# Kernel tuning notes

Hardware: AMD Instinct MI355X
Metric: run time of the kernel (lower is better)

Reference implementation:

```python
import jax, jax.numpy as jnp
import numpy as np

B, L, NIN, NHID, NLAYERS = 16, 2048, 1024, 1024, 2


def _gru_step_zero_h(x, W_ih, b_ih, W_hh, b_hh):
    """torch GRU cell with h_prev = 0 (faithful to the module's bug where
    hidden is never updated and starts at zeros).
    r = sigmoid(W_ir x + b_ir + b_hr)
    z = sigmoid(W_iz x + b_iz + b_hz)
    n = tanh(W_in x + b_in + r * b_hn)   # W_hn @ 0 == 0
    h = (1 - z) * n                       # + z * 0
    W_hh is unused because h_prev == 0 (kept as an arg for parity).
    """
    del W_hh
    g = jnp.einsum('blf,hf->blh', x, W_ih) + b_ih  # (B, L, 3H)
    H = b_ih.shape[0] // 3
    gi_r, gi_z, gi_n = g[..., :H], g[..., H:2 * H], g[..., 2 * H:]
    bh_r, bh_z, bh_n = b_hh[:H], b_hh[H:2 * H], b_hh[2 * H:]
    r = jax.nn.sigmoid(gi_r + bh_r)
    z = jax.nn.sigmoid(gi_z + bh_z)
    n = jnp.tanh(gi_n + r * bh_n)
    return (1.0 - z) * n


def setup_inputs() -> dict:
    key = jax.random.key(0)
    ks = jax.random.split(key, 12)
    s_in = 1.0 / np.sqrt(NIN)
    s_h = 1.0 / np.sqrt(NHID)
    inp = {
        'inputs': jax.random.normal(ks[0], (B, L, NIN), dtype=jnp.float32),
        'inputs_mask': jax.random.randint(ks[1], (B, L), 0, 2, dtype=jnp.int32),
        # layer 0 (input size NIN)
        'W_ih0': jax.random.uniform(ks[2], (3 * NHID, NIN), jnp.float32, -s_in, s_in),
        'W_hh0': jax.random.uniform(ks[3], (3 * NHID, NHID), jnp.float32, -s_h, s_h),
        'b_ih0': jax.random.uniform(ks[4], (3 * NHID,), jnp.float32, -s_h, s_h),
        'b_hh0': jax.random.uniform(ks[5], (3 * NHID,), jnp.float32, -s_h, s_h),
        # layer 1 (input size NHID)
        'W_ih1': jax.random.uniform(ks[6], (3 * NHID, NHID), jnp.float32, -s_h, s_h),
        'W_hh1': jax.random.uniform(ks[7], (3 * NHID, NHID), jnp.float32, -s_h, s_h),
        'b_ih1': jax.random.uniform(ks[8], (3 * NHID,), jnp.float32, -s_h, s_h),
        'b_hh1': jax.random.uniform(ks[9], (3 * NHID,), jnp.float32, -s_h, s_h),
    }
    return inp


def reference(inputs, inputs_mask, W_ih0, W_hh0, b_ih0, b_hh0,
              W_ih1, W_hh1, b_ih1, b_hh1):
    # hidden is never updated in the original step(), so every timestep runs
    # the 2-layer GRU one step from zero hidden -> fully parallel over time.
    h1 = _gru_step_zero_h(inputs, W_ih0, b_ih0, W_hh0, b_hh0)   # (B, L, H)
    h2 = _gru_step_zero_h(h1, W_ih1, b_ih1, W_hh1, b_hh1)       # (B, L, H)
    mask = inputs_mask.astype(h2.dtype)[..., None]               # (B, L, 1)
    # output_p * mask + hidden[0] * (1 - mask), with hidden[0] == 0
    out = h2 * mask
    # original returns (steps, b_s, nhid)
    return jnp.transpose(out, (1, 0, 2))
```

## Files before the change

### kernel.cpp

```cpp
#include <hip/hip_runtime.h>
#include <hip/hip_bf16.h>
#include <cstdint>
#include <cstddef>

#define BB 16
#define LL 2048
#define MM (BB * LL)
#define KK 1024
#define HH 1024

typedef __attribute__((ext_vector_type(8))) short bf16x8;
typedef __attribute__((ext_vector_type(4))) float f32x4;

__device__ __forceinline__ unsigned short f2bf(float f) {
    unsigned u = __builtin_bit_cast(unsigned, f);
    u += 0x7fffu + ((u >> 16) & 1u);
    return (unsigned short)(u >> 16);
}

__global__ void cvt_f32_to_bf16(const float* __restrict__ in,
                                unsigned short* __restrict__ out, int n8) {
    int i = blockIdx.x * blockDim.x + threadIdx.x;
    if (i >= n8) return;
    const float4* p = reinterpret_cast<const float4*>(in) + (size_t)i * 2;
    float4 v0 = p[0];
    float4 v1 = p[1];
    union { unsigned short us[8]; uint4 v; } o;
    o.us[0] = f2bf(v0.x); o.us[1] = f2bf(v0.y);
    o.us[2] = f2bf(v0.z); o.us[3] = f2bf(v0.w);
    o.us[4] = f2bf(v1.x); o.us[5] = f2bf(v1.y);
    o.us[6] = f2bf(v1.z); o.us[7] = f2bf(v1.w);
    reinterpret_cast<uint4*>(out)[i] = o.v;
}

__global__ __launch_bounds__(1024) void scan_mask(const int* __restrict__ mask,
                                                  int* __restrict__ rows,
                                                  int* __restrict__ Na) {
    __shared__ int psum[1024];
    const int t = threadIdx.x;
    const int base = t * 32;
    int m[32];
    int cnt = 0;
#pragma unroll
    for (int i = 0; i < 32; ++i) { m[i] = mask[base + i]; cnt += (m[i] != 0); }
    psum[t] = cnt;
    __syncthreads();
    for (int off = 1; off < 1024; off <<= 1) {
        int v = (t >= off) ? psum[t - off] : 0;
        __syncthreads();
        psum[t] += v;
        __syncthreads();
    }
    int offset = psum[t] - cnt;
#pragma unroll
    for (int i = 0; i < 32; ++i) {
        if (m[i]) rows[offset++] = base + i;
    }
    if (t == 1023) *Na = psum[1023];
}

__global__ __launch_bounds__(256) void gather_cvt(const float* __restrict__ x,
                                                  const int* __restrict__ rows,
                                                  const int* __restrict__ Na,
                                                  unsigned short* __restrict__ xbf) {
    const int j = blockIdx.x;
    if (j >= *Na) return;
    const int r = rows[j];
    const float4 v = reinterpret_cast<const float4*>(x + (size_t)r * KK)[threadIdx.x];
    ushort4 o;
    o.x = f2bf(v.x); o.y = f2bf(v.y); o.z = f2bf(v.z); o.w = f2bf(v.w);
    reinterpret_cast<ushort4*>(xbf + (size_t)j * KK)[threadIdx.x] = o;
}

__global__ __launch_bounds__(256) void zero_masked(const int* __restrict__ mask,
                                                   float* __restrict__ out) {
    const int m = blockIdx.x;
    if (mask[m] != 0) return;
    const int bb = m >> 11;
    const int ll = m & 2047;
    float4 z = {0.f, 0.f, 0.f, 0.f};
    reinterpret_cast<float4*>(out + ((size_t)ll * BB + bb) * HH)[threadIdx.x] = z;
}

__device__ __forceinline__ void gload16(const unsigned short* g, unsigned short* l) {
    __builtin_amdgcn_global_load_lds(
        (const __attribute__((address_space(1))) unsigned int*)g,
        (__attribute__((address_space(3))) unsigned int*)l,
        16, 0, 0);
}

#define WAITVM2 asm volatile("s_waitcnt vmcnt(2)" ::: "memory")
#define WAITVM7 asm volatile("s_waitcnt vmcnt(7)" ::: "memory")
#define WAITVM0 asm volatile("s_waitcnt vmcnt(0)" ::: "memory")
#define WAITLG0 asm volatile("s_waitcnt lgkmcnt(0)" ::: "memory")
#define SB      __builtin_amdgcn_sched_barrier(0)
#define BAR     __builtin_amdgcn_s_barrier()

template <int MODE>
__global__ __launch_bounds__(512, 2) void gru_layer(
    const unsigned short* __restrict__ A,
    const unsigned short* __restrict__ W,
    const float* __restrict__ b_ih,
    const float* __restrict__ b_hh,
    const int* __restrict__ rows,
    const int* __restrict__ Na_p,
    unsigned short* __restrict__ out_bf,
    float* __restrict__ out_f) {
    __shared__ unsigned short lds[2][28672];

    const int Na = *Na_p;
    const int m0 = blockIdx.x * 256;
    if (m0 >= Na) return;
    const int n0 = blockIdx.y * 64;

    const int tid  = threadIdx.x;
    const int lane = tid & 63;
    const int wid  = tid >> 6;
    const int wr   = wid >> 2;
    const int wc   = wid & 3;

    const int trow = tid >> 3;
    const int tcol = ((tid & 7) ^ (trow & 7)) * 8;
    int r0 = m0 + trow;        if (r0 >= Na) r0 = Na - 1;
    int r1 = m0 + 64 + trow;   if (r1 >= Na) r1 = Na - 1;
    int r2 = m0 + 128 + trow;  if (r2 >= Na) r2 = Na - 1;
    int r3 = m0 + 192 + trow;  if (r3 >= Na) r3 = Na - 1;
    const unsigned short* a0 = A + (size_t)r0 * KK + tcol;
    const unsigned short* a1 = A + (size_t)r1 * KK + tcol;
    const unsigned short* a2 = A + (size_t)r2 * KK + tcol;
    const unsigned short* a3 = A + (size_t)r3 * KK + tcol;
    const unsigned short* b0 = W + (size_t)(0 * HH + n0 + trow) * KK + tcol;
    const unsigned short* b1 = W + (size_t)(1 * HH + n0 + trow) * KK + tcol;
    const unsigned short* b2 = W + (size_t)(2 * HH + n0 + trow) * KK + tcol;

#define STAGE(kt, c) do {                                       \
        const int _o = (kt) * 64;                               \
        unsigned short* _L = &lds[(c)][wid * 512];              \
        gload16(a0 + _o, _L + 0 * 4096);                        \
        gload16(a2 + _o, _L + 2 * 4096);                        \
        gload16(b0 + _o, _L + 16384 + 0 * 4096);                \
        gload16(b1 + _o, _L + 16384 + 1 * 4096);                \
        gload16(b2 + _o, _L + 16384 + 2 * 4096);                \
        gload16(a1 + _o, _L + 1 * 4096);                        \
        gload16(a3 + _o, _L + 3 * 4096);                        \
    } while (0)

    const int l15  = lane & 15;
    const int akp0 = (((lane >> 4) << 3)) ^ ((lane & 7) << 3);
    const int akp1 = (32 + ((lane >> 4) << 3)) ^ ((lane & 7) << 3);
    int aoff0[4], aoff1[4], boff[3];
#pragma unroll
    for (int mf = 0; mf < 4; ++mf) {
        aoff0[mf] = (wr * 128 + 0 * 64 + mf * 16 + l15) * 64;
        aoff1[mf] = (wr * 128 + 1 * 64 + mf * 16 + l15) * 64;
    }
#pragma unroll
    for (int g = 0; g < 3; ++g)
        boff[g] = 16384 + g * 4096 + (wc * 16 + l15) * 64;

    f32x4 acc0[4][3] = {};
    f32x4 acc1[4][3] = {};
    bf16x8 afrag[4];
    bf16x8 bfrag[3];

#define READ_B(Lp, akp) do {                                                   \
        _Pragma("unroll") for (int g = 0; g < 3; ++g)                          \
            bfrag[g] = *reinterpret_cast<const bf16x8*>(&(Lp)[boff[g] + (akp)]); \
    } while (0)
#define READ_A0(Lp, akp) do {                                                   \
        _Pragma("unroll") for (int mf = 0; mf < 4; ++mf)                        \
            afrag[mf] = *reinterpret_cast<const bf16x8*>(&(Lp)[aoff0[mf] + (akp)]); \
    } while (0)
#define READ_A1(Lp, akp) do {                                                   \
        _Pragma("unroll") for (int mf = 0; mf < 4; ++mf)                        \
            afrag[mf] = *reinterpret_cast<const bf16x8*>(&(Lp)[aoff1[mf] + (akp)]); \
    } while (0)
#define PHASE_MFMA(accN) do {                                                   \
        __builtin_amdgcn_s_setprio(1);                                          \
        _Pragma("unroll") for (int g = 0; g < 3; ++g)                           \
            _Pragma("unroll") for (int mf = 0; mf < 4; ++mf)                    \
                accN[mf][g] = __builtin_amdgcn_mfma_f32_16x16x32_bf16(          \
                    afrag[mf], bfrag[g], accN[mf][g], 0, 0, 0);                 \
        __builtin_amdgcn_s_setprio(0);                                          \
    } while (0)

    STAGE(0, 0);

    int cur = 0;
#pragma unroll 1
    for (int kt = 0; kt < 15; ++kt) {
        unsigned short* L = &lds[cur][0];
        WAITVM2; BAR; SB;
        READ_B(L, akp0); READ_A0(L, akp0);
        STAGE(kt + 1, cur ^ 1);
        SB;
        WAITLG0; SB;
        PHASE_MFMA(acc0);
        WAITVM7; BAR; SB;
        READ_A1(L, akp0);
        WAITLG0; SB;
        PHASE_MFMA(acc1);
        READ_B(L, akp1); READ_A0(L, akp1);
        WAITLG0; SB;
        PHASE_MFMA(acc0);
        READ_A1(L, akp1);
        WAITLG0; SB;
        PHASE_MFMA(acc1);
        cur ^= 1;
    }
    {
        unsigned short* L = &lds[cur][0];
        WAITVM2; BAR; SB;
        READ_B(L, akp0); READ_A0(L, akp0);
        WAITLG0; SB;
        PHASE_MFMA(acc0);
        WAITVM0; BAR; SB;
        READ_A1(L, akp0);
        WAITLG0; SB;
        PHASE_MFMA(acc1);
        READ_B(L, akp1); READ_A0(L, akp1);
        WAITLG0; SB;
        PHASE_MFMA(acc0);
        READ_A1(L, akp1);
        WAITLG0; SB;
        PHASE_MFMA(acc1);
    }

    const int col = n0 + wc * 16 + l15;
    const float br_b = b_ih[col] + b_hh[col];
    const float bz_b = b_ih[HH + col] + b_hh[HH + col];
    const float bn_i = b_ih[2 * HH + col];
    const float bn_h = b_hh[2 * HH + col];

#define EPILOGUE(accN, mh) do {                                                  \
        _Pragma("unroll") for (int mf = 0; mf < 4; ++mf) {                       \
            _Pragma("unroll") for (int j = 0; j < 4; ++j) {                      \
                const int row = m0 + wr * 128 + (mh) * 64 + mf * 16 +            \
                                (lane >> 4) * 4 + j;                             \
                if (row < Na) {                                                  \
                    const float r = 1.f / (1.f + __expf(-(accN[mf][0][j] + br_b))); \
                    const float z = 1.f / (1.f + __expf(-(accN[mf][1][j] + bz_b))); \
                    const float n = tanhf(accN[mf][2][j] + bn_i + r * bn_h);     \
                    const float h = (1.f - z) * n;                               \
                    if (MODE == 0) {                                             \
                        out_bf[(size_t)row * HH + col] = f2bf(h);                \
                    } else {                                                     \
                        const int orig = rows[row];                              \
                        const int bb = orig >> 11;                               \
                        const int ll = orig & 2047;                              \
                        out_f[((size_t)ll * BB + bb) * HH + col] = h;            \
                    }                                                            \
                }                                                                \
            }                                                                    \
        }                                                                        \
    } while (0)

    EPILOGUE(acc0, 0);
    EPILOGUE(acc1, 1);
#undef STAGE
#undef READ_B
#undef READ_A0
#undef READ_A1
#undef PHASE_MFMA
#undef EPILOGUE
}

extern "C" void kernel_launch(void* const* d_in, const int* in_sizes, int n_in,
                              void* d_out, int out_size, void* d_ws, size_t ws_size,
                              hipStream_t stream) {
    const float* x   = (const float*)d_in[0];
    const int*   msk = (const int*)d_in[1];
    const float* W0  = (const float*)d_in[2];
    const float* bi0 = (const float*)d_in[4];
    const float* bh0 = (const float*)d_in[5];
    const float* W1  = (const float*)d_in[6];
    const float* bi1 = (const float*)d_in[8];
    const float* bh1 = (const float*)d_in[9];
    float* out = (float*)d_out;

    char* ws = (char*)d_ws;
    unsigned short* xbf  = (unsigned short*)ws;
    unsigned short* h1bf = (unsigned short*)(ws + 67108864);
    unsigned short* w0bf = (unsigned short*)(ws + 134217728);
    unsigned short* w1bf = (unsigned short*)(ws + 140509184);
    int* rows = (int*)(ws + 146800640);
    int* Na   = (int*)(ws + 146931712);

    scan_mask<<<1, 1024, 0, stream>>>(msk, rows, Na);

    cvt_f32_to_bf16<<<1536, 256, 0, stream>>>(W0, w0bf, 3 * HH * KK / 8);
    cvt_f32_to_bf16<<<1536, 256, 0, stream>>>(W1, w1bf, 3 * HH * KK / 8);

    zero_masked<<<MM, 256, 0, stream>>>(msk, out);
    gather_cvt<<<MM, 256, 0, stream>>>(x, rows, Na, xbf);

    dim3 grid(MM / 256, HH / 64);
    gru_layer<0><<<grid, 512, 0, stream>>>(xbf, w0bf, bi0, bh0, rows, Na, h1bf, nullptr);
    gru_layer<1><<<grid, 512, 0, stream>>>(h1bf, w1bf, bi1, bh1, rows, Na, nullptr, out);
}
```

Measured before the change: 416.6 us.

## Interleave global-to-LDS prefetch loads across MFMA phases with extra barriers

The GEMM main loop used to issue all seven next-tile global-to-LDS loads in one burst. They are now split into three groups (A0/A2, the three B tiles, A1/A3), each placed between a different MFMA phase. Extra workgroup barriers are added around the LDS reads, in a ping-pong style schedule that keeps waves in lockstep. The aim is to spread memory traffic across the compute phases. The cost is more s_barrier instructions per iteration, which may stall waves.

Result: no change. 419.4 us (+0.7%).

```diff
diff --git a/kernel.cpp b/kernel.cpp
--- a/kernel.cpp
+++ b/kernel.cpp
@@ -90,7 +90,6 @@
 }
 
 #define WAITVM2 asm volatile("s_waitcnt vmcnt(2)" ::: "memory")
-#define WAITVM7 asm volatile("s_waitcnt vmcnt(7)" ::: "memory")
 #define WAITVM0 asm volatile("s_waitcnt vmcnt(0)" ::: "memory")
 #define WAITLG0 asm volatile("s_waitcnt lgkmcnt(0)" ::: "memory")
 #define SB      __builtin_amdgcn_sched_barrier(0)
@@ -133,17 +132,7 @@
     const unsigned short* b1 = W + (size_t)(1 * HH + n0 + trow) * KK + tcol;
     const unsigned short* b2 = W + (size_t)(2 * HH + n0 + trow) * KK + tcol;
 
-#define STAGE(kt, c) do {                                       \
-        const int _o = (kt) * 64;                               \
-        unsigned short* _L = &lds[(c)][wid * 512];              \
-        gload16(a0 + _o, _L + 0 * 4096);                        \
-        gload16(a2 + _o, _L + 2 * 4096);                        \
-        gload16(b0 + _o, _L + 16384 + 0 * 4096);                \
-        gload16(b1 + _o, _L + 16384 + 1 * 4096);                \
-        gload16(b2 + _o, _L + 16384 + 2 * 4096);                \
-        gload16(a1 + _o, _L + 1 * 4096);                        \
-        gload16(a3 + _o, _L + 3 * 4096);                        \
-    } while (0)
+#define ST(ptr, kt, c, unit) gload16((ptr) + (kt) * 64, &lds[(c)][(unit) * 4096 + wid * 512])
 
     const int l15  = lane & 15;
     const int akp0 = (((lane >> 4) << 3)) ^ ((lane & 7) << 3);
@@ -163,16 +152,16 @@
     bf16x8 afrag[4];
     bf16x8 bfrag[3];
 
-#define READ_B(Lp, akp) do {                                                   \
-        _Pragma("unroll") for (int g = 0; g < 3; ++g)                          \
+#define READ_B(Lp, akp) do {                                                    \
+        _Pragma("unroll") for (int g = 0; g < 3; ++g)                           \
             bfrag[g] = *reinterpret_cast<const bf16x8*>(&(Lp)[boff[g] + (akp)]); \
     } while (0)
-#define READ_A0(Lp, akp) do {                                                   \
-        _Pragma("unroll") for (int mf = 0; mf < 4; ++mf)                        \
+#define READ_A0(Lp, akp) do {                                                    \
+        _Pragma("unroll") for (int mf = 0; mf < 4; ++mf)                         \
             afrag[mf] = *reinterpret_cast<const bf16x8*>(&(Lp)[aoff0[mf] + (akp)]); \
     } while (0)
-#define READ_A1(Lp, akp) do {                                                   \
-        _Pragma("unroll") for (int mf = 0; mf < 4; ++mf)                        \
+#define READ_A1(Lp, akp) do {                                                    \
+        _Pragma("unroll") for (int mf = 0; mf < 4; ++mf)                         \
             afrag[mf] = *reinterpret_cast<const bf16x8*>(&(Lp)[aoff1[mf] + (akp)]); \
     } while (0)
 #define PHASE_MFMA(accN) do {                                                   \
@@ -184,43 +173,54 @@
         __builtin_amdgcn_s_setprio(0);                                          \
     } while (0)
 
-    STAGE(0, 0);
+    ST(a0, 0, 0, 0); ST(a2, 0, 0, 2);
+    ST(b0, 0, 0, 4); ST(b1, 0, 0, 5); ST(b2, 0, 0, 6);
+    ST(a1, 0, 0, 1); ST(a3, 0, 0, 3);
+    WAITVM2; BAR;
 
     int cur = 0;
 #pragma unroll 1
     for (int kt = 0; kt < 15; ++kt) {
         unsigned short* L = &lds[cur][0];
-        WAITVM2; BAR; SB;
-        READ_B(L, akp0); READ_A0(L, akp0);
-        STAGE(kt + 1, cur ^ 1);
-        SB;
-        WAITLG0; SB;
+        const int nc = cur ^ 1;
+        READ_A0(L, akp0); READ_B(L, akp0);
+        ST(a0, kt + 1, nc, 0); ST(a2, kt + 1, nc, 2);
+        BAR; WAITLG0; SB;
         PHASE_MFMA(acc0);
-        WAITVM7; BAR; SB;
+        WAITVM2;
+        BAR;
         READ_A1(L, akp0);
-        WAITLG0; SB;
+        ST(b0, kt + 1, nc, 4); ST(b1, kt + 1, nc, 5); ST(b2, kt + 1, nc, 6);
+        BAR; WAITLG0; SB;
         PHASE_MFMA(acc1);
-        READ_B(L, akp1); READ_A0(L, akp1);
-        WAITLG0; SB;
+        BAR;
+        READ_A0(L, akp1); READ_B(L, akp1);
+        ST(a1, kt + 1, nc, 1); ST(a3, kt + 1, nc, 3);
+        BAR; WAITLG0; SB;
         PHASE_MFMA(acc0);
+        BAR;
         READ_A1(L, akp1);
-        WAITLG0; SB;
+        BAR; WAITLG0; SB;
         PHASE_MFMA(acc1);
+        WAITVM2;
+        BAR;
         cur ^= 1;
     }
     {
         unsigned short* L = &lds[cur][0];
-        WAITVM2; BAR; SB;
-        READ_B(L, akp0); READ_A0(L, akp0);
-        WAITLG0; SB;
+        READ_A0(L, akp0); READ_B(L, akp0);
+        BAR; WAITLG0; SB;
         PHASE_MFMA(acc0);
-        WAITVM0; BAR; SB;
+        WAITVM0;
+        BAR;
         READ_A1(L, akp0);
-        WAITLG0; SB;
+        BAR; WAITLG0; SB;
         PHASE_MFMA(acc1);
-        READ_B(L, akp1); READ_A0(L, akp1);
-        WAITLG0; SB;
+        BAR;
+        READ_A0(L, akp1); READ_B(L, akp1);
+        BAR; WAITLG0; SB;
         PHASE_MFMA(acc0);
+        BAR;
         READ_A1(L, akp1);
         WAITLG0; SB;
         PHASE_MFMA(acc1);
@@ -257,7 +257,7 @@
 
     EPILOGUE(acc0, 0);
     EPILOGUE(acc1, 1);
-#undef STAGE
+#undef ST
 #undef READ_B
 #undef READ_A0
 #undef READ_A1
```
